# Kernel tuning notes

Hardware: AMD Instinct MI355X
Metric: run time of the kernel (lower is better)

The kernel has to match this reference:

```python
import itertools
import jax, jax.numpy as jnp
import numpy as np

NUM_MOLS = 1024
N_ATOMS = 32  # atoms per molecule (< 50 per module's precomputed edge_indices)
Z_DIM = 64
HIDDEN = 256
NUM_ATOM_TYPES = 10
NUM_BOND_TYPES = 5  # hparams['num_bond_types'] + 1
BN_EPS = 1e-5


def _build_edge_index():
    base = np.array(list(itertools.combinations(range(N_ATOMS), 2)), dtype=np.int64)  # [496, 2]
    offsets = (N_ATOMS * np.arange(NUM_MOLS, dtype=np.int64))[:, None, None]
    return jnp.asarray((base[None] + offsets).reshape(-1, 2))  # [E, 2]


def setup_inputs() -> dict:
    key = jax.random.key(0)
    ks = jax.random.split(key, 4)
    total_atoms = NUM_MOLS * N_ATOMS
    return {
        "z": jax.random.normal(ks[0], (total_atoms, Z_DIM), dtype=jnp.float32),
        "W1": jax.random.normal(ks[1], (Z_DIM, HIDDEN), dtype=jnp.float32) * 0.05,
        "b1": jnp.zeros((HIDDEN,), jnp.float32),
        "bn_gamma": jnp.ones((HIDDEN,), jnp.float32),
        "bn_beta": jnp.zeros((HIDDEN,), jnp.float32),
        "W2": jax.random.normal(ks[2], (HIDDEN, NUM_ATOM_TYPES), dtype=jnp.float32) * 0.05,
        "b2": jnp.zeros((NUM_ATOM_TYPES,), jnp.float32),
        "bond_matrix": jax.random.normal(ks[3], (NUM_BOND_TYPES, Z_DIM, Z_DIM), dtype=jnp.float32),
        "edge_index": _build_edge_index(),
    }


def reference(z, W1, b1, bn_gamma, bn_beta, W2, b2, bond_matrix, edge_index):
    # atom classifier: Linear -> BatchNorm1d (training-mode batch stats) -> GELU -> Linear
    h = z @ W1 + b1  # [A, H]
    mean = jnp.mean(h, axis=0)
    var = jnp.mean((h - mean) ** 2, axis=0)  # biased variance, as torch BN
    h = (h - mean) * jax.lax.rsqrt(var + BN_EPS) * bn_gamma + bn_beta
    h = jax.nn.gelu(h, approximate=False)
    atom_types = h @ W2 + b2  # [A, num_atom_types]

    # symmetric bond matrices, per-edge bilinear quadratic form, softmax over bond types
    W = 0.5 * (bond_matrix + jnp.swapaxes(bond_matrix, 1, 2))  # [T, d, d]
    z1 = z[edge_index[:, 0]]  # [E, d]
    z2 = z[edge_index[:, 1]]  # [E, d]
    logits = jnp.einsum('ed,tdc,ec->et', z1, W, z2)  # [E, T]
    edge_types = jax.nn.softmax(logits, axis=1)
    return atom_types, edge_types
```

## Files before the change

kernel.cpp:

```cpp
#include <hip/hip_runtime.h>
#include <hip/hip_bf16.h>
#include <math.h>

#define NM 1024
#define NA 32
#define ZD 64
#define HD 256
#define AT 10
#define BT 5
#define NROWS (NM*NA)
#define EPM 496
#define ATOM_OUT (NROWS*AT)

__global__ __launch_bounds__(256) void k1_moments(const float* __restrict__ z,
                                                  float* __restrict__ Msum,
                                                  float* __restrict__ sumz) {
    __shared__ __align__(16) float zs[128][64];
    __shared__ float sred[4][64];
    const int tid = threadIdx.x;
    const int d0 = (tid >> 4) << 2;
    const int e0 = (tid & 15) << 2;
    const int d = tid & 63, rq = tid >> 6;
    float acc[4][4] = {};
    float colsum = 0.f;
    for (int chunk = 0; chunk < 4; ++chunk) {
        const int rowbase = (blockIdx.x * 4 + chunk) * 128;
        __syncthreads();
        for (int k = 0; k < 32; ++k) {
            int idx = tid + (k << 8);
            zs[idx >> 6][idx & 63] = z[rowbase * 64 + idx];
        }
        __syncthreads();
        for (int r = 0; r < 128; ++r) {
            float4 a4 = *(const float4*)&zs[r][d0];
            float4 b4 = *(const float4*)&zs[r][e0];
            float a[4] = {a4.x, a4.y, a4.z, a4.w};
            float b[4] = {b4.x, b4.y, b4.z, b4.w};
            #pragma unroll
            for (int i = 0; i < 4; ++i)
                #pragma unroll
                for (int jj = 0; jj < 4; ++jj) acc[i][jj] += a[i] * b[jj];
        }
        for (int r = rq * 32; r < rq * 32 + 32; ++r) colsum += zs[r][d];
    }
    #pragma unroll
    for (int i = 0; i < 4; ++i)
        #pragma unroll
        for (int jj = 0; jj < 4; ++jj)
            atomicAdd(&Msum[(d0 + i) * 64 + (e0 + jj)], acc[i][jj]);
    sred[rq][d] = colsum;
    __syncthreads();
    if (tid < 64)
        atomicAdd(&sumz[tid], sred[0][tid] + sred[1][tid] + sred[2][tid] + sred[3][tid]);
}

__global__ __launch_bounds__(256) void k2w(const float* __restrict__ Msum,
                                           const float* __restrict__ sumz,
                                           const float* __restrict__ W1,
                                           const float* __restrict__ gamma,
                                           const float* __restrict__ beta,
                                           const float* __restrict__ bond,
                                           float* __restrict__ avec,
                                           float* __restrict__ cvec,
                                           float* __restrict__ Wsym) {
    const int tid = threadIdx.x;
    if (blockIdx.x >= 64) {
        int idx = ((int)blockIdx.x - 64) * 256 + tid;
        int t = idx >> 12, rem = idx & 4095, dd = rem >> 6, c = rem & 63;
        Wsym[idx] = 0.5f * (bond[(t << 12) + (dd << 6) + c] +
                            bond[(t << 12) + (c << 6) + dd]);
        return;
    }
    const int wv = tid >> 6, d = tid & 63;
    const int j = blockIdx.x * 4 + wv;
    const float wdj = W1[d * HD + j];
    float v = 0.f;
    for (int e = 0; e < 64; ++e) v += Msum[d * 64 + e] * W1[e * HD + j];
    float q = v * wdj;
    float s = sumz[d] * wdj;
    #pragma unroll
    for (int off = 32; off >= 1; off >>= 1) {
        q += __shfl_down(q, off);
        s += __shfl_down(s, off);
    }
    if (d == 0) {
        const float invN = 1.f / (float)NROWS;
        float mean = s * invN;
        float var = q * invN - mean * mean;
        float a = gamma[j] * rsqrtf(var + 1e-5f);
        avec[j] = a;
        cvec[j] = beta[j] - mean * a;
    }
}

__global__ __launch_bounds__(256) void k3_mlp(const float* __restrict__ z,
                                              const float* __restrict__ W1,
                                              const float* __restrict__ W2,
                                              const float* __restrict__ b2,
                                              const float* __restrict__ avec,
                                              const float* __restrict__ cvec,
                                              float* __restrict__ out_atom) {
    __shared__ __align__(16) float zsT[64][68];
    __shared__ __align__(16) float w1s[16][256];
    __shared__ __align__(16) float w2s[256][10];
    __shared__ float as[256], cs[256];
    const int tid = threadIdx.x;
    const int rowbase = blockIdx.x * 64;
    for (int k = 0; k < 16; ++k) {
        int idx = tid + (k << 8);
        int r = idx >> 6, d = idx & 63;
        zsT[d][r] = z[(rowbase + r) * 64 + d];
    }
    for (int k = tid; k < HD * AT; k += 256) ((float*)w2s)[k] = W2[k];
    as[tid] = avec[tid]; cs[tid] = cvec[tid];

    const int rg = tid >> 4, cg = tid & 15;
    const int r0 = rg << 2;
    float acc[4][4][4] = {};
    for (int ch = 0; ch < 4; ++ch) {
        __syncthreads();
        for (int k = 0; k < 16; ++k) {
            int idx = tid + (k << 8);
            w1s[idx >> 8][idx & 255] = W1[(ch << 12) + idx];
        }
        __syncthreads();
        #pragma unroll
        for (int dl = 0; dl < 16; ++dl) {
            float4 zv = *(const float4*)&zsT[(ch << 4) + dl][r0];
            float zr[4] = {zv.x, zv.y, zv.z, zv.w};
            #pragma unroll
            for (int cb = 0; cb < 4; ++cb) {
                float4 wv = *(const float4*)&w1s[dl][(cb << 6) + (cg << 2)];
                float wr[4] = {wv.x, wv.y, wv.z, wv.w};
                #pragma unroll
                for (int ri = 0; ri < 4; ++ri)
                    #pragma unroll
                    for (int u = 0; u < 4; ++u) acc[ri][cb][u] += zr[ri] * wr[u];
            }
        }
    }
    float p[4][10] = {};
    #pragma unroll
    for (int cb = 0; cb < 4; ++cb)
        #pragma unroll
        for (int u = 0; u < 4; ++u) {
            const int c = (cb << 6) + (cg << 2) + u;
            const float a = as[c], cc = cs[c];
            #pragma unroll
            for (int ri = 0; ri < 4; ++ri) {
                float h = acc[ri][cb][u] * a + cc;
                h = 0.5f * h * (1.0f + erff(h * 0.70710678118654752f));
                #pragma unroll
                for (int o = 0; o < 10; ++o) p[ri][o] += h * w2s[c][o];
            }
        }
    #pragma unroll
    for (int m = 1; m <= 8; m <<= 1)
        #pragma unroll
        for (int ri = 0; ri < 4; ++ri)
            #pragma unroll
            for (int o = 0; o < 10; ++o) p[ri][o] += __shfl_xor(p[ri][o], m);
    if (cg == 0) {
        #pragma unroll
        for (int ri = 0; ri < 4; ++ri)
            for (int o = 0; o < 10; ++o)
                out_atom[(rowbase + r0 + ri) * AT + o] = p[ri][o] + b2[o];
    }
}

__global__ __launch_bounds__(256) void k4_edges(const float* __restrict__ z,
                                                const float* __restrict__ Wsym,
                                                float* __restrict__ out_edge) {
    __shared__ __align__(16) float zs[2][32][68];
    __shared__ __align__(16) float uT[2][5][32][36];
    const int tid = threadIdx.x;
    const int gmol0 = blockIdx.x * 2;
    for (int k = 0; k < 16; ++k) {
        int idx = tid + (k << 8);
        int ml = idx >> 11, rem = idx & 2047, j = rem >> 6, c = rem & 63;
        zs[ml][j][c] = z[((gmol0 + ml) * 32 + j) * 64 + c];
    }
    const int molB = tid >> 7, tid7 = tid & 127;
    const int i0 = (tid7 >> 4) << 2;
    const int j0 = (tid7 & 15) << 1;
    float accE[5][4][2] = {};
    const int wv = __builtin_amdgcn_readfirstlane(tid >> 6);
    const int lane = tid & 63;
    const int molA = lane >> 5, jA = lane & 31;
    __syncthreads();

    for (int dh = 0; dh < 2; ++dh) {
        const int d0 = dh * 32 + wv * 8;
        #pragma unroll
        for (int t = 0; t < 5; ++t) {
            float accA[8] = {};
            for (int cc = 0; cc < 16; ++cc) {
                float4 z4 = *(const float4*)&zs[molA][jA][cc << 2];
                float zr[4] = {z4.x, z4.y, z4.z, z4.w};
                #pragma unroll
                for (int k = 0; k < 4; ++k) {
                    const int c = (cc << 2) + k;
                    const float* wp = Wsym + ((t << 6) + c) * 64 + d0;
                    #pragma unroll
                    for (int dd = 0; dd < 8; ++dd) accA[dd] += wp[dd] * zr[k];
                }
            }
            #pragma unroll
            for (int dd = 0; dd < 8; ++dd) uT[molA][t][jA][wv * 8 + dd] = accA[dd];
        }
        __syncthreads();
        for (int q = 0; q < 8; ++q) {
            const int gd = dh * 32 + (q << 2);
            float zch[4][4];
            #pragma unroll
            for (int ri = 0; ri < 4; ++ri) {
                float4 zv = *(const float4*)&zs[molB][i0 + ri][gd];
                zch[ri][0] = zv.x; zch[ri][1] = zv.y; zch[ri][2] = zv.z; zch[ri][3] = zv.w;
            }
            #pragma unroll
            for (int t = 0; t < 5; ++t)
                #pragma unroll
                for (int rj = 0; rj < 2; ++rj) {
                    float4 uv = *(const float4*)&uT[molB][t][j0 + rj][q << 2];
                    float ur[4] = {uv.x, uv.y, uv.z, uv.w};
                    #pragma unroll
                    for (int ri = 0; ri < 4; ++ri)
                        #pragma unroll
                        for (int dd = 0; dd < 4; ++dd)
                            accE[t][ri][rj] += zch[ri][dd] * ur[dd];
                }
        }
        __syncthreads();
    }
    const int ebase = (gmol0 + molB) * EPM;
    #pragma unroll
    for (int ri = 0; ri < 4; ++ri)
        #pragma unroll
        for (int rj = 0; rj < 2; ++rj) {
            int i = i0 + ri, j = j0 + rj;
            if (i < j) {
                float l0 = accE[0][ri][rj], l1 = accE[1][ri][rj], l2 = accE[2][ri][rj];
                float l3 = accE[3][ri][rj], l4 = accE[4][ri][rj];
                float m = fmaxf(fmaxf(fmaxf(l0, l1), fmaxf(l2, l3)), l4);
                float e0 = expf(l0 - m), e1 = expf(l1 - m), e2 = expf(l2 - m);
                float e3 = expf(l3 - m), e4 = expf(l4 - m);
                float inv = 1.0f / (e0 + e1 + e2 + e3 + e4);
                int p = 31 * i - ((i * (i - 1)) >> 1) + (j - i - 1);
                float* o = out_edge + (ebase + p) * 5;
                o[0] = e0 * inv; o[1] = e1 * inv; o[2] = e2 * inv;
                o[3] = e3 * inv; o[4] = e4 * inv;
            }
        }
}

extern "C" void kernel_launch(void* const* d_in, const int* in_sizes, int n_in,
                              void* d_out, int out_size, void* d_ws, size_t ws_size,
                              hipStream_t stream) {
    (void)in_sizes; (void)n_in; (void)out_size; (void)ws_size;
    const float* z     = (const float*)d_in[0];
    const float* W1    = (const float*)d_in[1];
    const float* gamma = (const float*)d_in[3];
    const float* beta  = (const float*)d_in[4];
    const float* W2    = (const float*)d_in[5];
    const float* b2    = (const float*)d_in[6];
    const float* bond  = (const float*)d_in[7];
    float* out = (float*)d_out;
    float* ws  = (float*)d_ws;

    float* Msum = ws;
    float* sumz = ws + 4096;
    float* avec = ws + 4160;
    float* cvec = ws + 4416;
    float* Wsym = ws + 4672;

    hipMemsetAsync(ws, 0, (4096 + 64) * sizeof(float), stream);
    k1_moments<<<64, 256, 0, stream>>>(z, Msum, sumz);
    k2w<<<144, 256, 0, stream>>>(Msum, sumz, W1, gamma, beta, bond, avec, cvec, Wsym);
    k3_mlp<<<512, 256, 0, stream>>>(z, W1, W2, b2, avec, cvec, out);
    k4_edges<<<512, 256, 0, stream>>>(z, Wsym, out + ATOM_OUT);
}
```

Before: 237.0 us.

## Halve per-block work across kernels to raise grid size and occupancy

Each kernel now covers half as much data per block: k1 handles two 128-row chunks, k3 handles 32 rows, and k4 handles one molecule. The grids double to 128/1024/1024 blocks, launch bounds ask for 4 blocks per CU, and global loads become float4 vectorised. k4 is restructured so each lane holds half a z row in registers, computes the W·z projection in 16-column slices joined by a cross-half shuffle, and then does the i,j contraction with smaller shared buffers. The aim is better CU occupancy and latency hiding on a device with many CUs, at the cost of reloading W1/W2/Wsym in more blocks and adding more barriers to k4.

```diff
diff --git a/kernel.cpp b/kernel.cpp
--- a/kernel.cpp
+++ b/kernel.cpp
@@ -23,13 +23,13 @@
     const int d = tid & 63, rq = tid >> 6;
     float acc[4][4] = {};
     float colsum = 0.f;
-    for (int chunk = 0; chunk < 4; ++chunk) {
-        const int rowbase = (blockIdx.x * 4 + chunk) * 128;
-        __syncthreads();
-        for (int k = 0; k < 32; ++k) {
-            int idx = tid + (k << 8);
-            zs[idx >> 6][idx & 63] = z[rowbase * 64 + idx];
-        }
+    for (int chunk = 0; chunk < 2; ++chunk) {
+        const int rowbase = (blockIdx.x * 2 + chunk) * 128;
+        __syncthreads();
+        const float4* zg4 = (const float4*)(z + rowbase * 64);
+        float4* zs4 = (float4*)zs;
+        #pragma unroll
+        for (int k = 0; k < 8; ++k) zs4[tid + (k << 8)] = zg4[tid + (k << 8)];
         __syncthreads();
         for (int r = 0; r < 128; ++r) {
             float4 a4 = *(const float4*)&zs[r][d0];
@@ -93,53 +93,60 @@
     }
 }
 
-__global__ __launch_bounds__(256) void k3_mlp(const float* __restrict__ z,
-                                              const float* __restrict__ W1,
-                                              const float* __restrict__ W2,
-                                              const float* __restrict__ b2,
-                                              const float* __restrict__ avec,
-                                              const float* __restrict__ cvec,
-                                              float* __restrict__ out_atom) {
-    __shared__ __align__(16) float zsT[64][68];
+__global__ __launch_bounds__(256, 4) void k3_mlp(const float* __restrict__ z,
+                                                 const float* __restrict__ W1,
+                                                 const float* __restrict__ W2,
+                                                 const float* __restrict__ b2,
+                                                 const float* __restrict__ avec,
+                                                 const float* __restrict__ cvec,
+                                                 float* __restrict__ out_atom) {
+    __shared__ __align__(16) float zsT[64][36];
     __shared__ __align__(16) float w1s[16][256];
-    __shared__ __align__(16) float w2s[256][10];
+    __shared__ float w2s[256][11];
     __shared__ float as[256], cs[256];
     const int tid = threadIdx.x;
-    const int rowbase = blockIdx.x * 64;
-    for (int k = 0; k < 16; ++k) {
-        int idx = tid + (k << 8);
-        int r = idx >> 6, d = idx & 63;
-        zsT[d][r] = z[(rowbase + r) * 64 + d];
-    }
-    for (int k = tid; k < HD * AT; k += 256) ((float*)w2s)[k] = W2[k];
+    const int rowbase = blockIdx.x * 32;
+    {
+        const float* zp = z + (size_t)(rowbase + (tid >> 3)) * 64 + (tid & 7) * 8;
+        float4 v0 = *(const float4*)zp;
+        float4 v1 = *(const float4*)(zp + 4);
+        const int r = tid >> 3, dbase = (tid & 7) * 8;
+        zsT[dbase + 0][r] = v0.x; zsT[dbase + 1][r] = v0.y;
+        zsT[dbase + 2][r] = v0.z; zsT[dbase + 3][r] = v0.w;
+        zsT[dbase + 4][r] = v1.x; zsT[dbase + 5][r] = v1.y;
+        zsT[dbase + 6][r] = v1.z; zsT[dbase + 7][r] = v1.w;
+    }
+    for (int k = tid; k < HD * AT; k += 256) w2s[k / 10][k % 10] = W2[k];
     as[tid] = avec[tid]; cs[tid] = cvec[tid];
 
     const int rg = tid >> 4, cg = tid & 15;
-    const int r0 = rg << 2;
-    float acc[4][4][4] = {};
+    const int r0 = rg << 1;
+    float acc[2][4][4] = {};
     for (int ch = 0; ch < 4; ++ch) {
         __syncthreads();
+        #pragma unroll
         for (int k = 0; k < 16; ++k) {
             int idx = tid + (k << 8);
-            w1s[idx >> 8][idx & 255] = W1[(ch << 12) + idx];
+            ((float*)w1s)[idx] = W1[(ch << 12) + idx];
         }
         __syncthreads();
         #pragma unroll
         for (int dl = 0; dl < 16; ++dl) {
-            float4 zv = *(const float4*)&zsT[(ch << 4) + dl][r0];
-            float zr[4] = {zv.x, zv.y, zv.z, zv.w};
+            float zr0 = zsT[(ch << 4) + dl][r0];
+            float zr1 = zsT[(ch << 4) + dl][r0 + 1];
             #pragma unroll
             for (int cb = 0; cb < 4; ++cb) {
                 float4 wv = *(const float4*)&w1s[dl][(cb << 6) + (cg << 2)];
                 float wr[4] = {wv.x, wv.y, wv.z, wv.w};
                 #pragma unroll
-                for (int ri = 0; ri < 4; ++ri)
-                    #pragma unroll
-                    for (int u = 0; u < 4; ++u) acc[ri][cb][u] += zr[ri] * wr[u];
-            }
-        }
-    }
-    float p[4][10] = {};
+                for (int u = 0; u < 4; ++u) {
+                    acc[0][cb][u] += zr0 * wr[u];
+                    acc[1][cb][u] += zr1 * wr[u];
+                }
+            }
+        }
+    }
+    float p[2][10] = {};
     #pragma unroll
     for (int cb = 0; cb < 4; ++cb)
         #pragma unroll
@@ -147,7 +154,7 @@
             const int c = (cb << 6) + (cg << 2) + u;
             const float a = as[c], cc = cs[c];
             #pragma unroll
-            for (int ri = 0; ri < 4; ++ri) {
+            for (int ri = 0; ri < 2; ++ri) {
                 float h = acc[ri][cb][u] * a + cc;
                 h = 0.5f * h * (1.0f + erff(h * 0.70710678118654752f));
                 #pragma unroll
@@ -157,100 +164,115 @@
     #pragma unroll
     for (int m = 1; m <= 8; m <<= 1)
         #pragma unroll
-        for (int ri = 0; ri < 4; ++ri)
+        for (int ri = 0; ri < 2; ++ri)
             #pragma unroll
             for (int o = 0; o < 10; ++o) p[ri][o] += __shfl_xor(p[ri][o], m);
     if (cg == 0) {
         #pragma unroll
-        for (int ri = 0; ri < 4; ++ri)
+        for (int ri = 0; ri < 2; ++ri)
             for (int o = 0; o < 10; ++o)
-                out_atom[(rowbase + r0 + ri) * AT + o] = p[ri][o] + b2[o];
-    }
-}
-
-__global__ __launch_bounds__(256) void k4_edges(const float* __restrict__ z,
-                                                const float* __restrict__ Wsym,
-                                                float* __restrict__ out_edge) {
-    __shared__ __align__(16) float zs[2][32][68];
-    __shared__ __align__(16) float uT[2][5][32][36];
+                out_atom[(size_t)(rowbase + r0 + ri) * AT + o] = p[ri][o] + b2[o];
+    }
+}
+
+__global__ __launch_bounds__(256, 4) void k4_edges(const float* __restrict__ z,
+                                                   const float* __restrict__ Wsym,
+                                                   float* __restrict__ out_edge) {
+    __shared__ __align__(16) float zs[32][64];
+    __shared__ __align__(16) float uT[5][32][20];
     const int tid = threadIdx.x;
-    const int gmol0 = blockIdx.x * 2;
-    for (int k = 0; k < 16; ++k) {
-        int idx = tid + (k << 8);
-        int ml = idx >> 11, rem = idx & 2047, j = rem >> 6, c = rem & 63;
-        zs[ml][j][c] = z[((gmol0 + ml) * 32 + j) * 64 + c];
-    }
-    const int molB = tid >> 7, tid7 = tid & 127;
-    const int i0 = (tid7 >> 4) << 2;
-    const int j0 = (tid7 & 15) << 1;
-    float accE[5][4][2] = {};
-    const int wv = __builtin_amdgcn_readfirstlane(tid >> 6);
+    const int mol = blockIdx.x;
+    {
+        const float4* zg4 = (const float4*)(z + (size_t)mol * 2048);
+        float4* zs4 = (float4*)zs;
+        zs4[tid] = zg4[tid];
+        zs4[tid + 256] = zg4[tid + 256];
+    }
+    const int wv = tid >> 6;
     const int lane = tid & 63;
-    const int molA = lane >> 5, jA = lane & 31;
-    __syncthreads();
-
-    for (int dh = 0; dh < 2; ++dh) {
-        const int d0 = dh * 32 + wv * 8;
-        #pragma unroll
-        for (int t = 0; t < 5; ++t) {
-            float accA[8] = {};
-            for (int cc = 0; cc < 16; ++cc) {
-                float4 z4 = *(const float4*)&zs[molA][jA][cc << 2];
-                float zr[4] = {z4.x, z4.y, z4.z, z4.w};
-                #pragma unroll
-                for (int k = 0; k < 4; ++k) {
-                    const int c = (cc << 2) + k;
-                    const float* wp = Wsym + ((t << 6) + c) * 64 + d0;
-                    #pragma unroll
-                    for (int dd = 0; dd < 8; ++dd) accA[dd] += wp[dd] * zr[k];
+    const int jA = lane & 31;
+    const int ch = lane >> 5;
+    float zr[32];
+    {
+        const float* zrow = z + ((size_t)mol * 32 + jA) * 64 + ch * 32;
+        #pragma unroll
+        for (int k = 0; k < 8; ++k) {
+            float4 v = *(const float4*)(zrow + (k << 2));
+            zr[4 * k + 0] = v.x; zr[4 * k + 1] = v.y;
+            zr[4 * k + 2] = v.z; zr[4 * k + 3] = v.w;
+        }
+    }
+    const int jg = tid & 31;
+    const int ig = tid >> 5;
+    const int i0 = ig << 2;
+    float accE[5][4] = {};
+
+    for (int qd = 0; qd < 4; ++qd) {
+        float accA[5][4];
+        #pragma unroll
+        for (int t = 0; t < 5; ++t)
+            #pragma unroll
+            for (int dd = 0; dd < 4; ++dd) {
+                const float* wrow = Wsym + (size_t)((t << 6) + (qd << 4) + (wv << 2) + dd) * 64
+                                        + (ch << 5);
+                float a = 0.f;
+                #pragma unroll
+                for (int cc = 0; cc < 8; ++cc) {
+                    float4 w4 = *(const float4*)(wrow + (cc << 2));
+                    a += w4.x * zr[4 * cc] + w4.y * zr[4 * cc + 1]
+                       + w4.z * zr[4 * cc + 2] + w4.w * zr[4 * cc + 3];
                 }
-            }
-            #pragma unroll
-            for (int dd = 0; dd < 8; ++dd) uT[molA][t][jA][wv * 8 + dd] = accA[dd];
-        }
-        __syncthreads();
-        for (int q = 0; q < 8; ++q) {
-            const int gd = dh * 32 + (q << 2);
-            float zch[4][4];
+                accA[t][dd] = a;
+            }
+        #pragma unroll
+        for (int t = 0; t < 5; ++t)
+            #pragma unroll
+            for (int dd = 0; dd < 4; ++dd)
+                accA[t][dd] += __shfl_xor(accA[t][dd], 32);
+        __syncthreads();
+        if (ch == 0) {
+            #pragma unroll
+            for (int t = 0; t < 5; ++t) {
+                float4 w; w.x = accA[t][0]; w.y = accA[t][1];
+                w.z = accA[t][2]; w.w = accA[t][3];
+                *(float4*)&uT[t][jA][wv << 2] = w;
+            }
+        }
+        __syncthreads();
+        #pragma unroll
+        for (int cq = 0; cq < 4; ++cq) {
+            const int gd = (qd << 4) + (cq << 2);
+            float4 u4[5];
+            #pragma unroll
+            for (int t = 0; t < 5; ++t) u4[t] = *(const float4*)&uT[t][jg][cq << 2];
             #pragma unroll
             for (int ri = 0; ri < 4; ++ri) {
-                float4 zv = *(const float4*)&zs[molB][i0 + ri][gd];
-                zch[ri][0] = zv.x; zch[ri][1] = zv.y; zch[ri][2] = zv.z; zch[ri][3] = zv.w;
-            }
-            #pragma unroll
-            for (int t = 0; t < 5; ++t)
-                #pragma unroll
-                for (int rj = 0; rj < 2; ++rj) {
-                    float4 uv = *(const float4*)&uT[molB][t][j0 + rj][q << 2];
-                    float ur[4] = {uv.x, uv.y, uv.z, uv.w};
-                    #pragma unroll
-                    for (int ri = 0; ri < 4; ++ri)
-                        #pragma unroll
-                        for (int dd = 0; dd < 4; ++dd)
-                            accE[t][ri][rj] += zch[ri][dd] * ur[dd];
-                }
-        }
-        __syncthreads();
-    }
-    const int ebase = (gmol0 + molB) * EPM;
-    #pragma unroll
-    for (int ri = 0; ri < 4; ++ri)
-        #pragma unroll
-        for (int rj = 0; rj < 2; ++rj) {
-            int i = i0 + ri, j = j0 + rj;
-            if (i < j) {
-                float l0 = accE[0][ri][rj], l1 = accE[1][ri][rj], l2 = accE[2][ri][rj];
-                float l3 = accE[3][ri][rj], l4 = accE[4][ri][rj];
-                float m = fmaxf(fmaxf(fmaxf(l0, l1), fmaxf(l2, l3)), l4);
-                float e0 = expf(l0 - m), e1 = expf(l1 - m), e2 = expf(l2 - m);
-                float e3 = expf(l3 - m), e4 = expf(l4 - m);
-                float inv = 1.0f / (e0 + e1 + e2 + e3 + e4);
-                int p = 31 * i - ((i * (i - 1)) >> 1) + (j - i - 1);
-                float* o = out_edge + (ebase + p) * 5;
-                o[0] = e0 * inv; o[1] = e1 * inv; o[2] = e2 * inv;
-                o[3] = e3 * inv; o[4] = e4 * inv;
-            }
-        }
+                float4 zv = *(const float4*)&zs[i0 + ri][gd];
+                #pragma unroll
+                for (int t = 0; t < 5; ++t)
+                    accE[t][ri] += zv.x * u4[t].x + zv.y * u4[t].y
+                                 + zv.z * u4[t].z + zv.w * u4[t].w;
+            }
+        }
+        __syncthreads();
+    }
+    const int ebase = mol * EPM;
+    #pragma unroll
+    for (int ri = 0; ri < 4; ++ri) {
+        const int i = i0 + ri, j = jg;
+        if (i < j) {
+            float l0 = accE[0][ri], l1 = accE[1][ri], l2 = accE[2][ri];
+            float l3 = accE[3][ri], l4 = accE[4][ri];
+            float m = fmaxf(fmaxf(fmaxf(l0, l1), fmaxf(l2, l3)), l4);
+            float e0 = expf(l0 - m), e1 = expf(l1 - m), e2 = expf(l2 - m);
+            float e3 = expf(l3 - m), e4 = expf(l4 - m);
+            float inv = 1.0f / (e0 + e1 + e2 + e3 + e4);
+            int p = 31 * i - ((i * (i - 1)) >> 1) + (j - i - 1);
+            float* o = out_edge + (size_t)(ebase + p) * 5;
+            o[0] = e0 * inv; o[1] = e1 * inv; o[2] = e2 * inv;
+            o[3] = e3 * inv; o[4] = e4 * inv;
+        }
+    }
 }
 
 extern "C" void kernel_launch(void* const* d_in, const int* in_sizes, int n_in,
@@ -274,8 +296,8 @@
     float* Wsym = ws + 4672;
 
     hipMemsetAsync(ws, 0, (4096 + 64) * sizeof(float), stream);
-    k1_moments<<<64, 256, 0, stream>>>(z, Msum, sumz);
+    k1_moments<<<128, 256, 0, stream>>>(z, Msum, sumz);
     k2w<<<144, 256, 0, stream>>>(Msum, sumz, W1, gamma, beta, bond, avec, cvec, Wsym);
-    k3_mlp<<<512, 256, 0, stream>>>(z, W1, W2, b2, avec, cvec, out);
-    k4_edges<<<512, 256, 0, stream>>>(z, Wsym, out + ATOM_OUT);
-}
+    k3_mlp<<<1024, 256, 0, stream>>>(z, W1, W2, b2, avec, cvec, out);
+    k4_edges<<<1024, 256, 0, stream>>>(z, Wsym, out + ATOM_OUT);
+}
```

Result: slower. 370.8 us (+56.5%).
